# Performance work log

Measured on AMD Instinct MI355X. Metric: run time of the kernel, lower is better.

The kernel has to match this reference:

```python
import jax, jax.numpy as jnp
import numpy as np

B, I, H = 4096, 2048, 2048

def setup_inputs() -> dict:
    key = jax.random.key(0)
    ks = jax.random.split(key, 7)
    sk = (1.0 / H) ** 0.5
    return {
        "x": jax.random.normal(ks[0], (B, I), dtype=jnp.float32),
        "prev_state": jax.random.normal(ks[1], (B, H), dtype=jnp.float32),
        "c_state": jax.random.normal(ks[2], (B, H), dtype=jnp.float32),
        "W_fg": jax.random.uniform(ks[3], (H, H + I), jnp.float32, -sk, sk),
        "W_ig": jax.random.uniform(ks[4], (H, H + I), jnp.float32, -sk, sk),
        "W_og": jax.random.uniform(ks[5], (H, H + I), jnp.float32, -sk, sk),
        "W_ol": jax.random.uniform(ks[6], (H, H + I), jnp.float32, -sk, sk),
    }

def reference(x, prev_state, c_state, W_fg, W_ig, W_og, W_ol):
    # concat_hx: [B, H+I]
    concat_hx = jnp.concatenate([prev_state, x], axis=1)
    # Fuse the 4 gate GEMMs into one [B, H+I] x [H+I, 4H] matmul
    W_all = jnp.concatenate([W_fg, W_ig, W_og, W_ol], axis=0)  # [4H, H+I]
    gates = concat_hx @ W_all.T  # [B, 4H]
    ft, it, ct_t, ot = jnp.split(jax.nn.sigmoid(gates), 4, axis=1)
    # NOTE: original uses sigmoid (not tanh) for the candidate cell state ct_t
    ct = ft * c_state + it * ct_t
    ht = ot * jnp.tanh(ct)
    return ht
```

## Files before the change

kernel.cpp:

```cpp
#include <hip/hip_runtime.h>
#include <hip/hip_bf16.h>
#include <cstdint>
#include <cstddef>


typedef __bf16 nbf16;
typedef nbf16 bf16x8 __attribute__((ext_vector_type(8)));
typedef float f32x4 __attribute__((ext_vector_type(4)));

static constexpr int MDIM = 4096;
static constexpr int NDIM = 8192;
static constexpr int KDIM = 4096;
static constexpr int HDIM = 2048;
static constexpr int KB   = KDIM * 2;

#define VMW10 asm volatile("s_waitcnt vmcnt(10)" ::: "memory")
#define VMW0  asm volatile("s_waitcnt vmcnt(0)" ::: "memory")
#define LGKM0 asm volatile("s_waitcnt lgkmcnt(0)" ::: "memory")
#define LGKM4 asm volatile("s_waitcnt lgkmcnt(4)" ::: "memory")
#define LGKM8 asm volatile("s_waitcnt lgkmcnt(8)" ::: "memory")
#define BAR   __builtin_amdgcn_s_barrier()
#define SB0   __builtin_amdgcn_sched_barrier(0)
#define PRIO1 __builtin_amdgcn_s_setprio(1)
#define PRIO0 __builtin_amdgcn_s_setprio(0)

__device__ __forceinline__ void async16(void* lds, const void* g) {
    __builtin_amdgcn_global_load_lds(
        (const __attribute__((address_space(1))) void*)g,
        (__attribute__((address_space(3))) void*)lds,
        16, 0, 0);
}

__device__ __forceinline__ float fsig(float x) {
    return __builtin_amdgcn_rcpf(1.0f + __expf(-x));
}
__device__ __forceinline__ float ftanh(float x) {
    return 2.0f * __builtin_amdgcn_rcpf(1.0f + __expf(-2.0f * x)) - 1.0f;
}

__device__ __forceinline__ void stage_A(const char* Ab, int X, int t, char* slot,
                                        int wave, int r0, int cb) {
    const char* s = Ab + (size_t)(X * 64 + r0) * KB + t * 128 + cb;
    async16(slot + wave * 1024, s);
    async16(slot + (wave + 8) * 1024, s + (size_t)128 * KB);
}
__device__ __forceinline__ void stage_B(const char* Wb, int Y, int t, char* slot,
                                        int wave, int rB0, int cb) {
    const char* s = Wb + (size_t)(rB0 + Y * 32) * KB + t * 128 + cb;
    async16(slot + wave * 1024, s);
    async16(slot + (wave + 8) * 1024, s + (size_t)128 * KB);
}

__device__ __forceinline__ void read_A(bf16x8 (&d)[4][2], const char* hb,
                                       int ar, int kc0, int kc1) {
#pragma unroll
    for (int m = 0; m < 4; ++m) {
        d[m][0] = *(const bf16x8*)(hb + ar + m * 2048 + kc0);
        d[m][1] = *(const bf16x8*)(hb + ar + m * 2048 + kc1);
    }
}
__device__ __forceinline__ void read_B(bf16x8 (&d)[2][2], const char* hb,
                                       int br, int kc0, int kc1) {
#pragma unroll
    for (int j = 0; j < 2; ++j) {
        d[j][0] = *(const bf16x8*)(hb + br + j * 2048 + kc0);
        d[j][1] = *(const bf16x8*)(hb + br + j * 2048 + kc1);
    }
}
__device__ __forceinline__ void mfma16(f32x4 (&acc)[8][4], int mh, int Y,
                                       const bf16x8 (&a)[4][2],
                                       const bf16x8 (&b)[2][2]) {
#pragma unroll
    for (int m = 0; m < 4; ++m)
#pragma unroll
        for (int j = 0; j < 2; ++j) {
            acc[mh * 4 + m][Y * 2 + j] = __builtin_amdgcn_mfma_f32_16x16x32_bf16(
                a[m][0], b[j][0], acc[mh * 4 + m][Y * 2 + j], 0, 0, 0);
            acc[mh * 4 + m][Y * 2 + j] = __builtin_amdgcn_mfma_f32_16x16x32_bf16(
                a[m][1], b[j][1], acc[mh * 4 + m][Y * 2 + j], 0, 0, 0);
        }
}

__global__ __launch_bounds__(256) void k_concat_cast(
        const float* __restrict__ prev, const float* __restrict__ x,
        __hip_bfloat16* __restrict__ A) {
    const size_t total8 = (size_t)MDIM * KDIM / 8;
    const size_t stride = (size_t)gridDim.x * blockDim.x;
    for (size_t i = (size_t)blockIdx.x * blockDim.x + threadIdx.x; i < total8;
         i += stride) {
        size_t e = i * 8;
        size_t b = e >> 12;
        int k = (int)(e & (KDIM - 1));
        const float* src = (k < HDIM) ? (prev + b * HDIM + k)
                                      : (x + b * HDIM + (k - HDIM));
        float4 v0 = *(const float4*)src;
        float4 v1 = *(const float4*)(src + 4);
        union { __hip_bfloat16 h[8]; int4 q; } u;
        u.h[0] = __float2bfloat16(v0.x); u.h[1] = __float2bfloat16(v0.y);
        u.h[2] = __float2bfloat16(v0.z); u.h[3] = __float2bfloat16(v0.w);
        u.h[4] = __float2bfloat16(v1.x); u.h[5] = __float2bfloat16(v1.y);
        u.h[6] = __float2bfloat16(v1.z); u.h[7] = __float2bfloat16(v1.w);
        *(int4*)(A + e) = u.q;
    }
}

__global__ __launch_bounds__(256) void k_cast_w(
        const float* __restrict__ w0, const float* __restrict__ w1,
        const float* __restrict__ w2, const float* __restrict__ w3,
        __hip_bfloat16* __restrict__ W) {
    const size_t total8 = (size_t)NDIM * KDIM / 8;
    const size_t stride = (size_t)gridDim.x * blockDim.x;
    for (size_t i = (size_t)blockIdx.x * blockDim.x + threadIdx.x; i < total8;
         i += stride) {
        size_t e = i * 8;
        int n = (int)(e >> 12);
        int k = (int)(e & (KDIM - 1));
        int g = n & 3;
        size_t h = (size_t)(n >> 2);
        const float* src = (g == 0 ? w0 : g == 1 ? w1 : g == 2 ? w2 : w3)
                           + h * KDIM + k;
        float4 v0 = *(const float4*)src;
        float4 v1 = *(const float4*)(src + 4);
        union { __hip_bfloat16 h[8]; int4 q; } u;
        u.h[0] = __float2bfloat16(v0.x); u.h[1] = __float2bfloat16(v0.y);
        u.h[2] = __float2bfloat16(v0.z); u.h[3] = __float2bfloat16(v0.w);
        u.h[4] = __float2bfloat16(v1.x); u.h[5] = __float2bfloat16(v1.y);
        u.h[6] = __float2bfloat16(v1.z); u.h[7] = __float2bfloat16(v1.w);
        *(int4*)(W + e) = u.q;
    }
}

__global__ __launch_bounds__(512, 2) void k_gemm(
        const __hip_bfloat16* __restrict__ A, const __hip_bfloat16* __restrict__ W,
        const float* __restrict__ c, float* __restrict__ out) {
    __shared__ __align__(16) char lds[131072];

    const int bid = blockIdx.x;
    const int xcd = bid & 7, j = bid >> 3;
    const int mt = (xcd >> 2) * 8 + (j >> 3);
    const int nt = (xcd & 3) * 8 + (j & 7);
    const int brow = mt * 256, bcol = nt * 256;

    const int tid = threadIdx.x;
    const int wave = tid >> 6, lane = tid & 63;
    const int wr = wave >> 2, wc = wave & 3;

    const char* Ab = (const char*)A + (size_t)brow * KB;
    const char* Wb = (const char*)W + (size_t)bcol * KB;

    char* const Ah00 = lds;
    char* const Ah01 = lds + 16384;
    char* const Ah10 = lds + 32768;
    char* const Ah11 = lds + 49152;
    char* const Bh00 = lds + 65536;
    char* const Bh01 = lds + 81920;
    char* const Bh10 = lds + 98304;
    char* const Bh11 = lds + 114688;

    const int r0  = wave * 8 + (lane >> 3);
    const int rB0 = ((r0 >> 5) << 6) + (r0 & 31);
    const int cb  = (((lane & 7) ^ (lane >> 3)) << 4);
    const int kg  = lane >> 4;
    const int ar  = (wr * 64 + (lane & 15)) * 128;
    const int br  = (wc * 32 + (lane & 15)) * 128;
    const int kc0 = ((kg ^ (lane & 7)) << 4);
    const int kc1 = (((4 + kg) ^ (lane & 7)) << 4);

    f32x4 acc[8][4] = {};
    bf16x8 a0[4][2], a1[4][2], b0[2][2], b1[2][2];

    stage_B(Wb, 0, 0, Bh00, wave, rB0, cb);
    stage_A(Ab, 0, 0, Ah00, wave, r0, cb);
    stage_A(Ab, 1, 0, Ah01, wave, r0, cb);
    stage_B(Wb, 1, 0, Bh01, wave, rB0, cb);
    stage_B(Wb, 0, 1, Bh10, wave, rB0, cb);
    stage_A(Ab, 0, 1, Ah10, wave, r0, cb);
    stage_A(Ab, 1, 1, Ah11, wave, r0, cb);
    stage_B(Wb, 1, 1, Bh11, wave, rB0, cb);
    VMW10;
    SB0; BAR;
    read_A(a0, Ah00, ar, kc0, kc1);
    read_B(b0, Bh00, br, kc0, kc1);
    LGKM0;
    SB0; BAR;

    for (int i = 0; i < 32; ++i) {
        const int t2 = (2 * i + 2) & 63;
        const int t3 = (2 * i + 3) & 63;

        read_A(a1, Ah01, ar, kc0, kc1);
        stage_B(Wb, 0, t2, Bh00, wave, rB0, cb);
        VMW10; SB0; LGKM8; SB0;
        PRIO1; mfma16(acc, 0, 0, a0, b0); PRIO0;
        SB0; BAR;
        read_B(b1, Bh01, br, kc0, kc1);
        stage_A(Ab, 0, t2, Ah00, wave, r0, cb);
        VMW10; SB0; LGKM4; SB0;
        PRIO1; mfma16(acc, 1, 0, a1, b0); PRIO0;
        SB0; BAR;
        read_B(b0, Bh10, br, kc0, kc1);
        stage_A(Ab, 1, t2, Ah01, wave, r0, cb);
        VMW10; SB0; LGKM4; SB0;
        PRIO1; mfma16(acc, 1, 1, a1, b1); PRIO0;
        SB0; BAR;
        read_A(a1, Ah10, ar, kc0, kc1);
        stage_B(Wb, 1, t2, Bh01, wave, rB0, cb);
        VMW10; SB0; LGKM8; SB0;
        PRIO1; mfma16(acc, 0, 1, a0, b1); PRIO0;
        SB0; BAR;
        read_A(a0, Ah11, ar, kc0, kc1);
        stage_B(Wb, 0, t3, Bh10, wave, rB0, cb);
        VMW10; SB0; LGKM8; SB0;
        PRIO1; mfma16(acc, 0, 0, a1, b0); PRIO0;
        SB0; BAR;
        read_B(b1, Bh11, br, kc0, kc1);
        stage_A(Ab, 0, t3, Ah10, wave, r0, cb);
        VMW10; SB0; LGKM4; SB0;
        PRIO1; mfma16(acc, 1, 0, a0, b0); PRIO0;
        SB0; BAR;
        read_B(b0, Bh00, br, kc0, kc1);
        stage_A(Ab, 1, t3, Ah11, wave, r0, cb);
        VMW10; SB0; LGKM4; SB0;
        PRIO1; mfma16(acc, 1, 1, a0, b1); PRIO0;
        SB0; BAR;
        read_A(a0, Ah00, ar, kc0, kc1);
        stage_B(Wb, 1, t3, Bh11, wave, rB0, cb);
        VMW10; SB0; LGKM8; SB0;
        PRIO1; mfma16(acc, 0, 1, a1, b1); PRIO0;
        SB0; BAR;
    }

    VMW0; LGKM0;
    BAR;
    __hip_bfloat16* cl = (__hip_bfloat16*)lds;
    const int h0 = bcol >> 2;
    #pragma unroll
    for (int p = 0; p < 2; ++p) {
        if (p) BAR;
        if (wr == p) {
            const int rb = ((lane >> 4) << 2);
            const int cbase = wc * 64 + (lane & 15);
            #pragma unroll
            for (int mi = 0; mi < 8; ++mi)
                #pragma unroll
                for (int ni = 0; ni < 4; ++ni)
                    #pragma unroll
                    for (int q = 0; q < 4; ++q)
                        cl[(rb + mi * 16 + q) * 256 + (cbase + ni * 16)] =
                            __float2bfloat16(acc[mi][ni][q]);
        }
        BAR;
        #pragma unroll
        for (int rnd = 0; rnd < 4; ++rnd) {
            const int row = rnd * 32 + (tid >> 4);
            const int ccol = (tid & 15) * 16;
            union { int4 q[2]; __hip_bfloat16 h[16]; } v;
            v.q[0] = *(const int4*)&cl[row * 256 + ccol];
            v.q[1] = *(const int4*)&cl[row * 256 + ccol + 8];
            const size_t R = (size_t)(brow + p * 128 + row);
            const int hh = h0 + (tid & 15) * 4;
            float4 cc = *(const float4*)(c + R * HDIM + hh);
            float cs[4] = {cc.x, cc.y, cc.z, cc.w};
            float ht[4];
            #pragma unroll
            for (int u = 0; u < 4; ++u) {
                float ft  = fsig(__bfloat162float(v.h[4 * u + 0]));
                float it  = fsig(__bfloat162float(v.h[4 * u + 1]));
                float ctt = fsig(__bfloat162float(v.h[4 * u + 2]));
                float ot  = fsig(__bfloat162float(v.h[4 * u + 3]));
                float ct  = ft * cs[u] + it * ctt;
                ht[u] = ot * ftanh(ct);
            }
            float4 o = {ht[0], ht[1], ht[2], ht[3]};
            *(float4*)(out + R * HDIM + hh) = o;
        }
    }
}

extern "C" void kernel_launch(void* const* d_in, const int* in_sizes, int n_in,
                              void* d_out, int out_size, void* d_ws, size_t ws_size,
                              hipStream_t stream) {
    const float* x    = (const float*)d_in[0];
    const float* prev = (const float*)d_in[1];
    const float* cst  = (const float*)d_in[2];
    const float* wfg  = (const float*)d_in[3];
    const float* wig  = (const float*)d_in[4];
    const float* wog  = (const float*)d_in[5];
    const float* wol  = (const float*)d_in[6];
    float* out = (float*)d_out;

    char* ws = (char*)d_ws;
    __hip_bfloat16* Abf = (__hip_bfloat16*)(ws);
    __hip_bfloat16* Wbf = (__hip_bfloat16*)(ws + 33554432);

    k_concat_cast<<<2048, 256, 0, stream>>>(prev, x, Abf);
    k_cast_w<<<2048, 256, 0, stream>>>(wfg, wig, wog, wol, Wbf);
    k_gemm<<<512, 512, 0, stream>>>(Abf, Wbf, cst, out);
}
```

Before: 266.8 us.

## Restructure GEMM main loop into four phases with two MFMA blocks per barrier

The 8-phase main loop, which ran one MFMA quadrant per barrier, becomes 4 phases that each issue two LDS reads and two global-to-LDS stages, then run two MFMA quadrants before a single barrier. This halves the number of barriers and waitcnt points per K step, cutting synchronisation overhead and giving larger MFMA bursts between syncs. In exchange, more fragment registers are live at once and the vmcnt threshold changes to match the new issue pattern, so LDS read latency is now waited with a full lgkmcnt(0) after the MFMAs rather than overlapped partially.

```diff
diff --git a/kernel.cpp b/kernel.cpp
--- a/kernel.cpp
+++ b/kernel.cpp
@@ -14,11 +14,9 @@
 static constexpr int HDIM = 2048;
 static constexpr int KB   = KDIM * 2;
 
-#define VMW10 asm volatile("s_waitcnt vmcnt(10)" ::: "memory")
+#define VMW8  asm volatile("s_waitcnt vmcnt(8)" ::: "memory")
 #define VMW0  asm volatile("s_waitcnt vmcnt(0)" ::: "memory")
 #define LGKM0 asm volatile("s_waitcnt lgkmcnt(0)" ::: "memory")
-#define LGKM4 asm volatile("s_waitcnt lgkmcnt(4)" ::: "memory")
-#define LGKM8 asm volatile("s_waitcnt lgkmcnt(8)" ::: "memory")
 #define BAR   __builtin_amdgcn_s_barrier()
 #define SB0   __builtin_amdgcn_sched_barrier(0)
 #define PRIO1 __builtin_amdgcn_s_setprio(1)
@@ -167,7 +165,7 @@
     const int kc1 = (((4 + kg) ^ (lane & 7)) << 4);
 
     f32x4 acc[8][4] = {};
-    bf16x8 a0[4][2], a1[4][2], b0[2][2], b1[2][2];
+    bf16x8 A0[4][2], B0[2][2];
 
     stage_B(Wb, 0, 0, Bh00, wave, rB0, cb);
     stage_A(Ab, 0, 0, Ah00, wave, r0, cb);
@@ -177,57 +175,61 @@
     stage_A(Ab, 0, 1, Ah10, wave, r0, cb);
     stage_A(Ab, 1, 1, Ah11, wave, r0, cb);
     stage_B(Wb, 1, 1, Bh11, wave, rB0, cb);
-    VMW10;
+    VMW8;
     SB0; BAR;
-    read_A(a0, Ah00, ar, kc0, kc1);
-    read_B(b0, Bh00, br, kc0, kc1);
+    read_A(A0, Ah00, ar, kc0, kc1);
+    read_B(B0, Bh00, br, kc0, kc1);
     LGKM0;
     SB0; BAR;
 
     for (int i = 0; i < 32; ++i) {
         const int t2 = (2 * i + 2) & 63;
         const int t3 = (2 * i + 3) & 63;
-
-        read_A(a1, Ah01, ar, kc0, kc1);
+        bf16x8 aH[4][2], bH[2][2], A1[4][2], B1[2][2];
+
+        read_A(aH, Ah01, ar, kc0, kc1);
+        read_B(bH, Bh01, br, kc0, kc1);
         stage_B(Wb, 0, t2, Bh00, wave, rB0, cb);
-        VMW10; SB0; LGKM8; SB0;
-        PRIO1; mfma16(acc, 0, 0, a0, b0); PRIO0;
-        SB0; BAR;
-        read_B(b1, Bh01, br, kc0, kc1);
         stage_A(Ab, 0, t2, Ah00, wave, r0, cb);
-        VMW10; SB0; LGKM4; SB0;
-        PRIO1; mfma16(acc, 1, 0, a1, b0); PRIO0;
-        SB0; BAR;
-        read_B(b0, Bh10, br, kc0, kc1);
+        VMW8; SB0;
+        PRIO1;
+        mfma16(acc, 0, 0, A0, B0);
+        mfma16(acc, 1, 0, aH, B0);
+        PRIO0;
+        LGKM0; SB0; BAR;
+
+        read_B(B1, Bh10, br, kc0, kc1);
+        read_A(A1, Ah10, ar, kc0, kc1);
         stage_A(Ab, 1, t2, Ah01, wave, r0, cb);
-        VMW10; SB0; LGKM4; SB0;
-        PRIO1; mfma16(acc, 1, 1, a1, b1); PRIO0;
-        SB0; BAR;
-        read_A(a1, Ah10, ar, kc0, kc1);
         stage_B(Wb, 1, t2, Bh01, wave, rB0, cb);
-        VMW10; SB0; LGKM8; SB0;
-        PRIO1; mfma16(acc, 0, 1, a0, b1); PRIO0;
-        SB0; BAR;
-        read_A(a0, Ah11, ar, kc0, kc1);
+        VMW8; SB0;
+        PRIO1;
+        mfma16(acc, 1, 1, aH, bH);
+        mfma16(acc, 0, 1, A0, bH);
+        PRIO0;
+        LGKM0; SB0; BAR;
+
+        read_A(aH, Ah11, ar, kc0, kc1);
+        read_B(bH, Bh11, br, kc0, kc1);
         stage_B(Wb, 0, t3, Bh10, wave, rB0, cb);
-        VMW10; SB0; LGKM8; SB0;
-        PRIO1; mfma16(acc, 0, 0, a1, b0); PRIO0;
-        SB0; BAR;
-        read_B(b1, Bh11, br, kc0, kc1);
         stage_A(Ab, 0, t3, Ah10, wave, r0, cb);
-        VMW10; SB0; LGKM4; SB0;
-        PRIO1; mfma16(acc, 1, 0, a0, b0); PRIO0;
-        SB0; BAR;
-        read_B(b0, Bh00, br, kc0, kc1);
+        VMW8; SB0;
+        PRIO1;
+        mfma16(acc, 0, 0, A1, B1);
+        mfma16(acc, 1, 0, aH, B1);
+        PRIO0;
+        LGKM0; SB0; BAR;
+
+        read_B(B0, Bh00, br, kc0, kc1);
+        read_A(A0, Ah00, ar, kc0, kc1);
         stage_A(Ab, 1, t3, Ah11, wave, r0, cb);
-        VMW10; SB0; LGKM4; SB0;
-        PRIO1; mfma16(acc, 1, 1, a0, b1); PRIO0;
-        SB0; BAR;
-        read_A(a0, Ah00, ar, kc0, kc1);
         stage_B(Wb, 1, t3, Bh11, wave, rB0, cb);
-        VMW10; SB0; LGKM8; SB0;
-        PRIO1; mfma16(acc, 0, 1, a1, b1); PRIO0;
-        SB0; BAR;
+        VMW8; SB0;
+        PRIO1;
+        mfma16(acc, 1, 1, aH, bH);
+        mfma16(acc, 0, 1, A1, bH);
+        PRIO0;
+        LGKM0; SB0; BAR;
     }
 
     VMW0; LGKM0;
```

Measured after the change: 753.5 us. 182% more time.
